# Kernel optimization log

Hardware: AMD Instinct MI355X
Metric: run time of the kernel (lower is better)

The kernel has to match this reference:

```python
import jax, jax.numpy as jnp
import numpy as np
from jax import lax

# ---- geometry (from Mamba2PoSTMixer defaults + chosen d_model) ----
D_MODEL = 1024
EXPAND = 2
HEADDIM = 64
D_STATE = 128
D_CONV = 4
CHUNK = 256
D_INNER = EXPAND * D_MODEL            # 2048
NHEADS = D_INNER // HEADDIM           # 32
D_CONV_CH = D_INNER + 2 * D_STATE     # conv acts on x, B, C
D_IN_PROJ = 2 * D_INNER + 2 * D_STATE + NHEADS
BATCH, SEQLEN = 2, 4096
EPS = 1e-5


def setup_inputs() -> dict:
    key = jax.random.key(0)
    ks = jax.random.split(key, 8)
    f = jnp.float32
    return {
        "hidden_states": jax.random.normal(ks[0], (BATCH, SEQLEN, D_MODEL), f),
        "residual": jax.random.normal(ks[1], (BATCH, SEQLEN, D_MODEL), f),
        "norm_weight": jnp.ones((D_MODEL,), f),
        "in_proj_w": jax.random.normal(ks[2], (D_MODEL, D_IN_PROJ), f) * 0.02,
        "conv_w": jax.random.normal(ks[3], (D_CONV, 1, D_CONV_CH), f) * 0.2,  # WIO, depthwise
        "conv_b": jnp.zeros((D_CONV_CH,), f),
        "dt_bias": jnp.log(jnp.expm1(jax.random.uniform(ks[4], (NHEADS,), f, 1e-3, 1e-1))),
        "A_log": jnp.log(jax.random.uniform(ks[5], (NHEADS,), f, 1.0, 16.0)),
        "D": jnp.ones((NHEADS,), f),
        "gate_norm_weight": jnp.ones((D_INNER,), f),
        "out_proj_w": jax.random.normal(ks[6], (D_INNER, D_MODEL), f) * 0.02,
    }


def _rmsnorm(x, w, eps=EPS):
    return x * lax.rsqrt(jnp.mean(x * x, axis=-1, keepdims=True) + eps) * w


def _segsum(x):
    # x: [..., T] -> [..., T, T] lower-triangular cumulative segment sums
    T = x.shape[-1]
    cs = jnp.cumsum(x, axis=-1)
    ss = cs[..., :, None] - cs[..., None, :]
    mask = jnp.tril(jnp.ones((T, T), bool))
    return jnp.where(mask, ss, -jnp.inf)


def _ssd(xdt, dtA, Bm, Cm):
    # xdt: [b,l,h,p] (x already scaled by dt), dtA: [b,l,h], Bm/Cm: [b,l,n]
    b, l, h, p = xdt.shape
    n = Bm.shape[-1]
    c = l // CHUNK
    x = xdt.reshape(b, c, CHUNK, h, p)
    A = dtA.reshape(b, c, CHUNK, h).transpose(0, 3, 1, 2)     # [b,h,c,l]
    Bc = Bm.reshape(b, c, CHUNK, n)
    Cc = Cm.reshape(b, c, CHUNK, n)
    A_cum = jnp.cumsum(A, axis=-1)                            # [b,h,c,l]
    # intra-chunk (diagonal block) output
    L = jnp.exp(_segsum(A))                                   # [b,h,c,l,s]
    Y_diag = jnp.einsum('bcln,bcsn,bhcls,bcshp->bclhp', Cc, Bc, L, x)
    # per-chunk final states
    decay_states = jnp.exp(A_cum[..., -1:] - A_cum)           # [b,h,c,l]
    states = jnp.einsum('bcln,bhcl,bclhp->bchpn', Bc, decay_states, x)
    # inter-chunk recurrence over chunk states
    chunk_decay = jnp.exp(A_cum[..., -1])                     # [b,h,c]
    def step(carry, inp):
        dec, s = inp                                          # dec: [b,h], s: [b,h,p,n]
        return carry * dec[..., None, None] + s, carry
    init = jnp.zeros((b, h, p, n), xdt.dtype)
    _, prev = lax.scan(step, init,
                       (jnp.moveaxis(chunk_decay, -1, 0), jnp.moveaxis(states, 1, 0)))
    prev = jnp.moveaxis(prev, 0, 1)                           # [b,c,h,p,n] states entering each chunk
    Y_off = jnp.einsum('bcln,bchpn,bhcl->bclhp', Cc, prev, jnp.exp(A_cum))
    return (Y_diag + Y_off).reshape(b, l, h, p)


def reference(hidden_states, residual, norm_weight, in_proj_w, conv_w, conv_b,
              dt_bias, A_log, D, gate_norm_weight, out_proj_w):
    # residual add + RMSNorm (Mamba2PoSTBlock)
    res = hidden_states + residual
    h = _rmsnorm(res, norm_weight)
    # Mamba2 mixer
    zxbcdt = h @ in_proj_w                                    # [b,l, 2*Di + 2*N + H]
    z, xBC, dt_raw = jnp.split(zxbcdt, [D_INNER, D_INNER + D_CONV_CH], axis=-1)
    # depthwise causal conv over (x, B, C) channels + SiLU
    xp = jnp.pad(xBC, ((0, 0), (D_CONV - 1, 0), (0, 0)))
    xBC = lax.conv_general_dilated(xp, conv_w, (1,), 'VALID',
                                   dimension_numbers=('NWC', 'WIO', 'NWC'),
                                   feature_group_count=D_CONV_CH) + conv_b
    xBC = jax.nn.silu(xBC)
    x, Bm, Cm = jnp.split(xBC, [D_INNER, D_INNER + D_STATE], axis=-1)
    dt = jax.nn.softplus(dt_raw + dt_bias)                    # [b,l,H]
    A = -jnp.exp(A_log)                                       # [H]
    xh = x.reshape(x.shape[0], x.shape[1], NHEADS, HEADDIM)   # [b,l,h,p]
    y = _ssd(xh * dt[..., None], dt * A, Bm, Cm)
    y = y + D[None, None, :, None] * xh                       # skip (D) term
    y = y.reshape(y.shape[0], y.shape[1], D_INNER)
    y = _rmsnorm(y * jax.nn.silu(z), gate_norm_weight)        # gated RMSNorm
    out = y @ out_proj_w
    return out, res
```

## Files before the change

kernel.cpp:

```cpp
#include <hip/hip_runtime.h>
#include <hip/hip_bf16.h>
#include <math.h>

#define BATCH   2
#define LQ      4096
#define RTOT    8192
#define DM      1024
#define DI      2048
#define NH      32
#define HD      64
#define DS      128
#define CH      256
#define NC      16
#define XBC_C   2304
#define ZX_C    4384
#define ZXS     4352
#define NP1     4480
#define EPS     1e-5f
#define LOG2E   1.4426950408889634f

typedef __hip_bfloat16 bf16;
typedef __bf16 bf16x8v __attribute__((ext_vector_type(8)));
typedef __bf16 bf16x4v __attribute__((ext_vector_type(4)));
typedef float f32x4v __attribute__((ext_vector_type(4)));

__device__ __forceinline__ float block_reduce_sum(float v) {
    __shared__ float sred[8];
    int lane = threadIdx.x & 63, w = threadIdx.x >> 6;
#pragma unroll
    for (int off = 32; off > 0; off >>= 1) v += __shfl_down(v, off, 64);
    if (lane == 0) sred[w] = v;
    __syncthreads();
    float t = (threadIdx.x < (int)(blockDim.x >> 6)) ? sred[threadIdx.x] : 0.f;
    if (w == 0) {
#pragma unroll
        for (int off = 4; off > 0; off >>= 1) t += __shfl_down(t, off, 64);
        if (lane == 0) sred[0] = t;
    }
    __syncthreads();
    return sred[0];
}

__device__ __forceinline__ void transpose_tile(
    const float* __restrict__ W, bf16* __restrict__ WT, int K, int N,
    int n0, int k0) {
    __shared__ float t[32][33];
    int tx = threadIdx.x & 31, ty = threadIdx.x >> 5;
#pragma unroll
    for (int r = 0; r < 32; r += 8) {
        int k = k0 + ty + r, n = n0 + tx;
        t[ty + r][tx] = (n < N) ? W[(size_t)k * N + n] : 0.f;
    }
    __syncthreads();
#pragma unroll
    for (int r = 0; r < 32; r += 8) {
        int n = n0 + ty + r, k = k0 + tx;
        WT[(size_t)n * K + k] = __float2bfloat16(t[tx][ty + r]);
    }
}

__global__ __launch_bounds__(256) void fused_pre_kernel(
    const float* __restrict__ hid, const float* __restrict__ resid,
    const float* __restrict__ w, float* __restrict__ res_out,
    bf16* __restrict__ h_out, const float* __restrict__ in_proj,
    bf16* __restrict__ Bt1) {
    int bid = blockIdx.x;
    if (bid < RTOT) {
        int r = bid, tid = threadIdx.x;
        size_t base = (size_t)r * DM;
        float4 hv = *(const float4*)&hid[base + tid * 4];
        float4 rv = *(const float4*)&resid[base + tid * 4];
        float4 s = {hv.x + rv.x, hv.y + rv.y, hv.z + rv.z, hv.w + rv.w};
        *(float4*)&res_out[base + tid * 4] = s;
        float ss = s.x * s.x + s.y * s.y + s.z * s.z + s.w * s.w;
        ss = block_reduce_sum(ss);
        float scale = rsqrtf(ss / (float)DM + EPS);
        float4 wv = *(const float4*)&w[tid * 4];
        __hip_bfloat162 p0, p1;
        p0.x = __float2bfloat16(s.x * scale * wv.x);
        p0.y = __float2bfloat16(s.y * scale * wv.y);
        p1.x = __float2bfloat16(s.z * scale * wv.z);
        p1.y = __float2bfloat16(s.w * scale * wv.w);
        bf16* hp = &h_out[base + tid * 4];
        *(__hip_bfloat162*)hp = p0;
        *(__hip_bfloat162*)(hp + 2) = p1;
    } else {
        int t = bid - RTOT;
        transpose_tile(in_proj, Bt1, DM, ZX_C, (t % 140) * 32, (t / 140) * 32);
    }
}

template <int WRITE_F32>
__global__ __launch_bounds__(256) void gemm_mfma_kernel(
    const bf16* __restrict__ A, int lda, const bf16* __restrict__ Bt,
    void* __restrict__ C, int ldc, int M, int N, int K,
    float* __restrict__ dtraw) {
    __shared__ __align__(16) bf16 As[128 * 32];
    __shared__ __align__(16) bf16 Bs[128 * 32];
    int tid = threadIdx.x;
    int lane = tid & 63, wave = tid >> 6;
    int wm = (wave >> 1) * 64, wn = (wave & 1) * 64;
    int m0 = blockIdx.y * 128, n0 = blockIdx.x * 128;
    int fr = lane & 15, kg = lane >> 4;

    int off0 = tid * 16, off1 = off0 + 4096;
    int row0 = off0 >> 6, colb0 = off0 & 63;
    int row1 = off1 >> 6, colb1 = off1 & 63;
    const bf16* ga0 = A + (size_t)(m0 + row0) * lda + (colb0 >> 1);
    const bf16* ga1 = A + (size_t)(m0 + row1) * lda + (colb1 >> 1);
    const bf16* gb0 = Bt + (size_t)(n0 + row0) * K + (colb0 >> 1);
    const bf16* gb1 = Bt + (size_t)(n0 + row1) * K + (colb1 >> 1);

    f32x4v acc[4][4] = {};
    for (int k0 = 0; k0 < K; k0 += 32) {
        __syncthreads();
        __builtin_amdgcn_global_load_lds(
            (const __attribute__((address_space(1))) void*)(ga0 + k0),
            (__attribute__((address_space(3))) void*)((char*)As + off0), 16, 0, 0);
        __builtin_amdgcn_global_load_lds(
            (const __attribute__((address_space(1))) void*)(ga1 + k0),
            (__attribute__((address_space(3))) void*)((char*)As + off1), 16, 0, 0);
        __builtin_amdgcn_global_load_lds(
            (const __attribute__((address_space(1))) void*)(gb0 + k0),
            (__attribute__((address_space(3))) void*)((char*)Bs + off0), 16, 0, 0);
        __builtin_amdgcn_global_load_lds(
            (const __attribute__((address_space(1))) void*)(gb1 + k0),
            (__attribute__((address_space(3))) void*)((char*)Bs + off1), 16, 0, 0);
        __syncthreads();
        bf16x8v af[4], bfv[4];
#pragma unroll
        for (int mt = 0; mt < 4; ++mt)
            af[mt] = *(const bf16x8v*)&As[(wm + mt * 16 + fr) * 32 + kg * 8];
#pragma unroll
        for (int nt = 0; nt < 4; ++nt)
            bfv[nt] = *(const bf16x8v*)&Bs[(wn + nt * 16 + fr) * 32 + kg * 8];
#pragma unroll
        for (int mt = 0; mt < 4; ++mt)
#pragma unroll
            for (int nt = 0; nt < 4; ++nt)
                acc[mt][nt] = __builtin_amdgcn_mfma_f32_16x16x32_bf16(
                    af[mt], bfv[nt], acc[mt][nt], 0, 0, 0);
    }
    int col = lane & 15, rbase = (lane >> 4) * 4;
#pragma unroll
    for (int mt = 0; mt < 4; ++mt) {
#pragma unroll
        for (int nt = 0; nt < 4; ++nt) {
            int gn = n0 + wn + nt * 16 + col;
            if (gn >= N) continue;
#pragma unroll
            for (int rg = 0; rg < 4; ++rg) {
                int gm = m0 + wm + mt * 16 + rbase + rg;
                float v = acc[mt][nt][rg];
                if (WRITE_F32) {
                    ((float*)C)[(size_t)gm * ldc + gn] = v;
                } else {
                    if (gn < 4352)
                        ((bf16*)C)[(size_t)gm * ldc + gn] = __float2bfloat16(v);
                    else if (dtraw)
                        dtraw[(size_t)gm * 32 + (gn - 4352)] = v;
                }
            }
        }
    }
}

__global__ __launch_bounds__(256) void fused_conv_dt_kernel(
    const bf16* __restrict__ zx, const float* __restrict__ conv_w,
    const float* __restrict__ conv_b, bf16* __restrict__ xBC,
    const float* __restrict__ dtraw, const float* __restrict__ dt_bias,
    const float* __restrict__ A_log, float* __restrict__ dt_bh,
    float* __restrict__ Ac2_bh) {
    int bid = blockIdx.x;
    if (bid < 9216) {
        int idx = bid * 256 + threadIdx.x;
        int r = idx / 288;
        int o = idx - r * 288;
        int c = o * 8;
        int b = r >> 12, l = r & (LQ - 1);
        float acc[8];
        {
            float4 cb0 = *(const float4*)&conv_b[c];
            float4 cb1 = *(const float4*)&conv_b[c + 4];
            acc[0] = cb0.x; acc[1] = cb0.y; acc[2] = cb0.z; acc[3] = cb0.w;
            acc[4] = cb1.x; acc[5] = cb1.y; acc[6] = cb1.z; acc[7] = cb1.w;
        }
#pragma unroll
        for (int k = 0; k < 4; ++k) {
            int t = l - 3 + k;
            if (t >= 0) {
                bf16x8v xv = *(const bf16x8v*)&zx[(size_t)(b * LQ + t) * ZXS + DI + c];
                float4 w0 = *(const float4*)&conv_w[k * XBC_C + c];
                float4 w1 = *(const float4*)&conv_w[k * XBC_C + c + 4];
                acc[0] = fmaf(w0.x, (float)xv[0], acc[0]);
                acc[1] = fmaf(w0.y, (float)xv[1], acc[1]);
                acc[2] = fmaf(w0.z, (float)xv[2], acc[2]);
                acc[3] = fmaf(w0.w, (float)xv[3], acc[3]);
                acc[4] = fmaf(w1.x, (float)xv[4], acc[4]);
                acc[5] = fmaf(w1.y, (float)xv[5], acc[5]);
                acc[6] = fmaf(w1.z, (float)xv[6], acc[6]);
                acc[7] = fmaf(w1.w, (float)xv[7], acc[7]);
            }
        }
        bf16x8v ov;
#pragma unroll
        for (int j = 0; j < 8; ++j)
            ov[j] = (__bf16)(acc[j] / (1.f + __expf(-acc[j])));
        *(bf16x8v*)&xBC[(size_t)r * XBC_C + c] = ov;
    } else {
        __shared__ float sA[256];
        int b2 = bid - 9216;
        int c = b2 & 15, h = (b2 >> 4) & 31, b = b2 >> 9;
        int tid = threadIdx.x;
        int l = c * CH + tid;
        int r = b * LQ + l;
        float v = dtraw[(size_t)r * 32 + h] + dt_bias[h];
        float dt = (v > 20.f) ? v : log1pf(expf(v));
        float A = -expf(A_log[h]);
        sA[tid] = dt * A * LOG2E;
        __syncthreads();
        for (int off = 1; off < 256; off <<= 1) {
            float t = (tid >= off) ? sA[tid - off] : 0.f;
            __syncthreads();
            sA[tid] += t;
            __syncthreads();
        }
        size_t o = (size_t)(b * NH + h) * LQ + l;
        dt_bh[o] = dt;
        Ac2_bh[o] = sA[tid];
    }
}

__global__ __launch_bounds__(256) void states_mfma_kernel(
    const bf16* __restrict__ xBC, const float* __restrict__ dt_bh,
    const float* __restrict__ Ac2, float* __restrict__ states) {
    __shared__ __align__(16) __bf16 xdT[64][264];
    __shared__ __align__(16) __bf16 BT[64][264];
    int bid = blockIdx.x;
    int c = bid & 15, h = (bid >> 4) & 31, b = bid >> 9;
    int bh = b * NH + h;
    int rch = b * LQ + c * CH;
    int tid = threadIdx.x;
    int wave = tid >> 6, lane = tid & 63;
    int fr = lane & 15, kg = lane >> 4;
    float Ac2last = Ac2[(size_t)bh * LQ + c * CH + (CH - 1)];

    {
        int p2 = (tid & 31) * 2;
        int srow = tid >> 5;
#pragma unroll 4
        for (int pass = 0; pass < 32; ++pass) {
            int s = pass * 8 + srow;
            float sc = dt_bh[(size_t)bh * LQ + c * CH + s] *
                       exp2f(Ac2last - Ac2[(size_t)bh * LQ + c * CH + s]);
            __hip_bfloat162 xv =
                *(const __hip_bfloat162*)&xBC[(size_t)(rch + s) * XBC_C + h * HD + p2];
            xdT[p2][s]     = (__bf16)(__bfloat162float(xv.x) * sc);
            xdT[p2 + 1][s] = (__bf16)(__bfloat162float(xv.y) * sc);
        }
    }
    int wm = (wave >> 1) * 32, wn = (wave & 1) * 32;
    size_t base = (size_t)(bh * NC + c) * HD * DS;
    for (int nh = 0; nh < 2; ++nh) {
        __syncthreads();
        {
            int n_oct = tid & 7, lrow = tid >> 3;
#pragma unroll
            for (int pass = 0; pass < 8; ++pass) {
                int l = pass * 32 + lrow;
                bf16x8v bv = *(const bf16x8v*)
                    &xBC[(size_t)(rch + l) * XBC_C + DI + nh * 64 + n_oct * 8];
#pragma unroll
                for (int j = 0; j < 8; ++j)
                    BT[n_oct * 8 + j][l] = bv[j];
            }
        }
        __syncthreads();
        f32x4v acc[2][2] = {};
#pragma unroll
        for (int kb = 0; kb < 8; ++kb) {
            bf16x8v A2[2], B2[2];
#pragma unroll
            for (int i = 0; i < 2; ++i)
                A2[i] = *(const bf16x8v*)&xdT[wm + i * 16 + fr][kb * 32 + kg * 8];
#pragma unroll
            for (int j = 0; j < 2; ++j)
                B2[j] = *(const bf16x8v*)&BT[wn + j * 16 + fr][kb * 32 + kg * 8];
#pragma unroll
            for (int i = 0; i < 2; ++i)
#pragma unroll
                for (int j = 0; j < 2; ++j)
                    acc[i][j] = __builtin_amdgcn_mfma_f32_16x16x32_bf16(
                        A2[i], B2[j], acc[i][j], 0, 0, 0);
        }
#pragma unroll
        for (int i = 0; i < 2; ++i)
#pragma unroll
            for (int j = 0; j < 2; ++j)
#pragma unroll
                for (int rg = 0; rg < 4; ++rg) {
                    int p = wm + i * 16 + kg * 4 + rg;
                    int n = nh * 64 + wn + j * 16 + fr;
                    states[base + (size_t)p * DS + n] = acc[i][j][rg];
                }
    }
}

__global__ __launch_bounds__(256) void chunk_scan_kernel(
    float* __restrict__ states, const float* __restrict__ Ac2) {
    int bh = blockIdx.x;
    int tid = threadIdx.x;
    float carry[32];
#pragma unroll
    for (int j = 0; j < 32; ++j) carry[j] = 0.f;
    for (int c = 0; c < NC; ++c) {
        float dec = exp2f(Ac2[(size_t)bh * LQ + c * CH + (CH - 1)]);
        size_t base = (size_t)(bh * NC + c) * (HD * DS);
#pragma unroll
        for (int j = 0; j < 32; ++j) {
            size_t idx = base + tid + j * 256;
            float tmp = states[idx];
            states[idx] = carry[j];
            carry[j] = carry[j] * dec + tmp;
        }
    }
}

template <int MASKED>
__device__ __forceinline__ void y_slab(
    const bf16* __restrict__ xBC, int rch, int s0, int fr, int kg,
    const float* As_sh, const float* Al, const bf16x8v CA[4][4],
    __bf16 (*Pw)[36], const __bf16 (*xdtT)[264], f32x4v accY[4][4]) {
#pragma unroll
    for (int half = 0; half < 2; ++half) {
        f32x4v Sacc[2][4] = {};
#pragma unroll
        for (int ks = 0; ks < 4; ++ks) {
            bf16x8v SB[2];
#pragma unroll
            for (int st2 = 0; st2 < 2; ++st2)
                SB[st2] = *(const bf16x8v*)&xBC[
                    (size_t)(rch + s0 + half * 32 + st2 * 16 + fr) * XBC_C
                    + DI + ks * 32 + kg * 8];
#pragma unroll
            for (int st2 = 0; st2 < 2; ++st2)
#pragma unroll
                for (int mt = 0; mt < 4; ++mt) {
                    if (MASKED && (half * 2 + st2) > mt) continue;
                    Sacc[st2][mt] = __builtin_amdgcn_mfma_f32_16x16x32_bf16(
                        SB[st2], CA[mt][ks], Sacc[st2][mt], 0, 0, 0);
                }
        }
#pragma unroll
        for (int st2 = 0; st2 < 2; ++st2) {
            int sblk = half * 2 + st2;
            float4 As4 = *(const float4*)&As_sh[s0 + half * 32 + st2 * 16 + kg * 4];
            float as[4] = {As4.x, As4.y, As4.z, As4.w};
#pragma unroll
            for (int mt = 0; mt < 4; ++mt) {
                bf16x4v pv;
                if (MASKED && sblk > mt) {
                    pv[0] = pv[1] = pv[2] = pv[3] = (__bf16)0.f;
                } else {
#pragma unroll
                    for (int rg = 0; rg < 4; ++rg) {
                        float v = Sacc[st2][mt][rg] * exp2f(Al[mt] - as[rg]);
                        if (MASKED && sblk == mt && (kg * 4 + rg) > fr) v = 0.f;
                        pv[rg] = (__bf16)v;
                    }
                }
                *(bf16x4v*)&Pw[mt * 16 + fr][st2 * 16 + kg * 4] = pv;
            }
        }
        __asm__ volatile("s_waitcnt lgkmcnt(0)" ::: "memory");
        bf16x8v PA[4], XB[4];
#pragma unroll
        for (int mt = 0; mt < 4; ++mt) {
            bf16x4v plo = *(const bf16x4v*)&Pw[mt * 16 + fr][kg * 8];
            bf16x4v phi = *(const bf16x4v*)&Pw[mt * 16 + fr][kg * 8 + 4];
            bf16x8v pa;
#pragma unroll
            for (int j = 0; j < 4; ++j) { pa[j] = plo[j]; pa[4 + j] = phi[j]; }
            PA[mt] = pa;
        }
#pragma unroll
        for (int pt = 0; pt < 4; ++pt)
            XB[pt] = *(const bf16x8v*)&xdtT[pt * 16 + fr][s0 + half * 32 + kg * 8];
#pragma unroll
        for (int mt = 0; mt < 4; ++mt)
#pragma unroll
            for (int pt = 0; pt < 4; ++pt)
                accY[mt][pt] = __builtin_amdgcn_mfma_f32_16x16x32_bf16(
                    PA[mt], XB[pt], accY[mt][pt], 0, 0, 0);
        __asm__ volatile("s_waitcnt lgkmcnt(0)" ::: "memory");
    }
}

__global__ __launch_bounds__(256) void y_mfma_kernel(
    const bf16* __restrict__ xBC, const float* __restrict__ dt_bh,
    const float* __restrict__ Ac2, const float* __restrict__ prev,
    bf16* __restrict__ yout ) {
    __shared__ __align__(16) __bf16 xdtT[64][264];
    __shared__ __align__(16) __bf16 P[4][64][36];
    __shared__ float As_sh[256];
    int bid = blockIdx.x;
    int c = bid & 15, h = (bid >> 4) & 31, b = bid >> 9;
    int bh = b * NH + h;
    int rch = b * LQ + c * CH;
    int tid = threadIdx.x;
    int wave = tid >> 6, lane = tid & 63;
    int fr = lane & 15, kg = lane >> 4;

    As_sh[tid] = Ac2[(size_t)bh * LQ + c * CH + tid];
    {
        int p2 = (tid & 31) * 2;
        int srow = tid >> 5;
#pragma unroll 4
        for (int pass = 0; pass < 32; ++pass) {
            int s = pass * 8 + srow;
            float dtv = dt_bh[(size_t)bh * LQ + c * CH + s];
            __hip_bfloat162 xv =
                *(const __hip_bfloat162*)&xBC[(size_t)(rch + s) * XBC_C + h * HD + p2];
            xdtT[p2][s]     = (__bf16)(__bfloat162float(xv.x) * dtv);
            xdtT[p2 + 1][s] = (__bf16)(__bfloat162float(xv.y) * dtv);
        }
    }
    __syncthreads();

    bf16x8v CA[4][4];
    {
        size_t rb = (size_t)(rch + wave * 64 + fr) * XBC_C + DI + DS + kg * 8;
#pragma unroll
        for (int mt = 0; mt < 4; ++mt)
#pragma unroll
            for (int ks = 0; ks < 4; ++ks)
                CA[mt][ks] = *(const bf16x8v*)&xBC[rb + (size_t)mt * 16 * XBC_C + ks * 32];
    }

    f32x4v accY[4][4] = {};

    {
        size_t pbase = (size_t)(bh * NC + c) * HD * DS;
#pragma unroll
        for (int ks = 0; ks < 4; ++ks) {
            bf16x8v PB[4];
#pragma unroll
            for (int pt = 0; pt < 4; ++pt) {
                const float* pp = &prev[pbase + (size_t)(pt * 16 + fr) * DS + ks * 32 + kg * 8];
                float4 a4 = *(const float4*)pp;
                float4 b4 = *(const float4*)(pp + 4);
                bf16x8v t;
                t[0] = (__bf16)a4.x; t[1] = (__bf16)a4.y; t[2] = (__bf16)a4.z; t[3] = (__bf16)a4.w;
                t[4] = (__bf16)b4.x; t[5] = (__bf16)b4.y; t[6] = (__bf16)b4.z; t[7] = (__bf16)b4.w;
                PB[pt] = t;
            }
#pragma unroll
            for (int mt = 0; mt < 4; ++mt)
#pragma unroll
                for (int pt = 0; pt < 4; ++pt)
                    accY[mt][pt] = __builtin_amdgcn_mfma_f32_16x16x32_bf16(
                        CA[mt][ks], PB[pt], accY[mt][pt], 0, 0, 0);
        }
    }
    int l0 = wave * 64;
#pragma unroll
    for (int mt = 0; mt < 4; ++mt) {
#pragma unroll
        for (int rg = 0; rg < 4; ++rg) {
            float e = exp2f(As_sh[l0 + mt * 16 + kg * 4 + rg]);
#pragma unroll
            for (int pt = 0; pt < 4; ++pt)
                accY[mt][pt][rg] *= e;
        }
    }

    float Al[4];
#pragma unroll
    for (int mt = 0; mt < 4; ++mt) Al[mt] = As_sh[l0 + mt * 16 + fr];

    __bf16 (*Pw)[36] = P[wave];
    for (int st = 0; st < wave; ++st)
        y_slab<0>(xBC, rch, st * 64, fr, kg, As_sh, Al, CA, Pw, xdtT, accY);
    y_slab<1>(xBC, rch, l0, fr, kg, As_sh, Al, CA, Pw, xdtT, accY);

#pragma unroll
    for (int ph = 0; ph < 2; ++ph) {
#pragma unroll
        for (int mt = 0; mt < 4; ++mt)
#pragma unroll
            for (int ptl = 0; ptl < 2; ++ptl)
#pragma unroll
                for (int rg = 0; rg < 4; ++rg)
                    Pw[mt * 16 + kg * 4 + rg][ptl * 16 + fr] =
                        (__bf16)accY[mt][ph * 2 + ptl][rg];
        __asm__ volatile("s_waitcnt lgkmcnt(0)" ::: "memory");
        bf16* yp = yout + (size_t)(rch + l0 + lane) * ZXS + h * HD + ph * 32;
#pragma unroll
        for (int q = 0; q < 4; ++q) {
            bf16x4v a = *(const bf16x4v*)&Pw[lane][q * 8];
            bf16x4v bq = *(const bf16x4v*)&Pw[lane][q * 8 + 4];
            bf16x8v v;
#pragma unroll
            for (int j = 0; j < 4; ++j) { v[j] = a[j]; v[4 + j] = bq[j]; }
            *(bf16x8v*)(yp + q * 8) = v;
        }
        __asm__ volatile("s_waitcnt lgkmcnt(0)" ::: "memory");
    }
}

__global__ __launch_bounds__(256) void fused_gate_trans_kernel(
    const bf16* __restrict__ zx, const float* __restrict__ gw,
    const float* __restrict__ Dvec, const bf16* __restrict__ xBC,
    bf16* __restrict__ y ,
    const float* __restrict__ out_proj, bf16* __restrict__ Bt2) {
    int bid = blockIdx.x;
    if (bid < RTOT) {
        int r = bid, tid = threadIdx.x;
        int i0 = tid * 8;
        bf16x8v zv = *(const bf16x8v*)&zx[(size_t)r * ZXS + i0];
        bf16x8v yv = *(const bf16x8v*)&y[(size_t)r * ZXS + i0];
        bf16x8v xv = *(const bf16x8v*)&xBC[(size_t)r * XBC_C + i0];
        float Dh = Dvec[tid >> 3];
        float v[8];
        float ss = 0.f;
#pragma unroll
        for (int j = 0; j < 8; ++j) {
            float z = (float)zv[j];
            float val = ((float)yv[j] + Dh * (float)xv[j]) * (z / (1.f + __expf(-z)));
            v[j] = val;
            ss += val * val;
        }
        ss = block_reduce_sum(ss);
        float scale = rsqrtf(ss / (float)DI + EPS);
        float4 g0 = *(const float4*)&gw[i0];
        float4 g1 = *(const float4*)&gw[i0 + 4];
        float g[8] = {g0.x, g0.y, g0.z, g0.w, g1.x, g1.y, g1.z, g1.w};
        bf16x8v ov;
#pragma unroll
        for (int j = 0; j < 8; ++j)
            ov[j] = (__bf16)(v[j] * scale * g[j]);
        *(bf16x8v*)&y[(size_t)r * ZXS + i0] = ov;
    } else {
        int t = bid - RTOT;
        transpose_tile(out_proj, Bt2, DI, DM, (t & 31) * 32, (t >> 5) * 32);
    }
}

extern "C" void kernel_launch(void* const* d_in, const int* in_sizes, int n_in,
                              void* d_out, int out_size, void* d_ws, size_t ws_size,
                              hipStream_t stream) {
    const float* hid      = (const float*)d_in[0];
    const float* resid    = (const float*)d_in[1];
    const float* norm_w   = (const float*)d_in[2];
    const float* in_proj  = (const float*)d_in[3];
    const float* conv_w   = (const float*)d_in[4];
    const float* conv_b   = (const float*)d_in[5];
    const float* dt_bias  = (const float*)d_in[6];
    const float* A_log    = (const float*)d_in[7];
    const float* Dvec     = (const float*)d_in[8];
    const float* gate_w   = (const float*)d_in[9];
    const float* out_proj = (const float*)d_in[10];

    float* out_p   = (float*)d_out;
    float* res_out = out_p + (size_t)RTOT * DM;
    bf16*  h_bf16  = (bf16*)out_p;
    float* states  = out_p;

    char* wsb = (char*)d_ws;
    bf16*  zx      = (bf16*)wsb;  wsb += (size_t)RTOT * ZXS * sizeof(bf16);
    bf16*  xBC     = (bf16*)wsb;  wsb += (size_t)RTOT * XBC_C * sizeof(bf16);
    float* dtraw   = (float*)wsb; wsb += (size_t)RTOT * 32 * sizeof(float);
    float* dt_bh   = (float*)wsb; wsb += (size_t)BATCH * NH * LQ * sizeof(float);
    float* Ac2_bh  = (float*)wsb; wsb += (size_t)BATCH * NH * LQ * sizeof(float);
    wsb += (size_t)1 << 20;
    bf16* Bt1 = xBC;
    bf16* Bt2 = (bf16*)dtraw;

    fused_pre_kernel<<<RTOT + 4480, 256, 0, stream>>>(
        hid, resid, norm_w, res_out, h_bf16, in_proj, Bt1);
    gemm_mfma_kernel<0><<<dim3(NP1 / 128, RTOT / 128), 256, 0, stream>>>(
        h_bf16, DM, Bt1, zx, ZXS, RTOT, ZX_C, DM, dtraw);
    fused_conv_dt_kernel<<<9216 + 1024, 256, 0, stream>>>(
        zx, conv_w, conv_b, xBC, dtraw, dt_bias, A_log, dt_bh, Ac2_bh);
    states_mfma_kernel<<<BATCH * NH * NC, 256, 0, stream>>>(
        xBC, dt_bh, Ac2_bh, states);
    chunk_scan_kernel<<<BATCH * NH, 256, 0, stream>>>(states, Ac2_bh);
    y_mfma_kernel<<<BATCH * NH * NC, 256, 0, stream>>>(
        xBC, dt_bh, Ac2_bh, states, zx + DI);
    fused_gate_trans_kernel<<<RTOT + 2048, 256, 0, stream>>>(
        zx, gate_w, Dvec, xBC, zx + DI, out_proj, Bt2);
    gemm_mfma_kernel<1><<<dim3(DM / 128, RTOT / 128), 256, 0, stream>>>(
        zx + DI, ZXS, Bt2, out_p, DM, RTOT, DM, DI, nullptr);
}
```

Baseline: 529.8 us.

## Replace GEMM with 256-row, 8-wave, double-buffered, swizzled 8-phase pipelined MFMA kernel

Both projection GEMMs move from a simple 128x128 tile kernel, which synchronises twice per 32-wide K step, to a 256xBN tile kernel with 512 threads. It double-buffers 64-wide K tiles in LDS with XOR-swizzled layout and interleaves async global-to-LDS loads with MFMA phases under explicit waitcnt and barrier control. It also raises MFMA priority and swizzles the block order for L2 reuse. The in_proj N padding grows to 4608, so the transpose and grid sizes change, and a bounds check guards the dtraw writes. The aim is better MFMA utilisation and latency hiding, at the cost of higher LDS and register use and fragile hand-tuned vmcnt counts.

```diff
diff --git a/kernel.cpp b/kernel.cpp
--- a/kernel.cpp
+++ b/kernel.cpp
@@ -15,7 +15,7 @@
 #define XBC_C   2304
 #define ZX_C    4384
 #define ZXS     4352
-#define NP1     4480
+#define NP1     4608
 #define EPS     1e-5f
 #define LOG2E   1.4426950408889634f
 
@@ -86,78 +86,174 @@
         *(__hip_bfloat162*)(hp + 2) = p1;
     } else {
         int t = bid - RTOT;
-        transpose_tile(in_proj, Bt1, DM, ZX_C, (t % 140) * 32, (t / 140) * 32);
-    }
-}
-
-template <int WRITE_F32>
-__global__ __launch_bounds__(256) void gemm_mfma_kernel(
-    const bf16* __restrict__ A, int lda, const bf16* __restrict__ Bt,
-    void* __restrict__ C, int ldc, int M, int N, int K,
-    float* __restrict__ dtraw) {
-    __shared__ __align__(16) bf16 As[128 * 32];
-    __shared__ __align__(16) bf16 Bs[128 * 32];
-    int tid = threadIdx.x;
-    int lane = tid & 63, wave = tid >> 6;
-    int wm = (wave >> 1) * 64, wn = (wave & 1) * 64;
-    int m0 = blockIdx.y * 128, n0 = blockIdx.x * 128;
-    int fr = lane & 15, kg = lane >> 4;
-
-    int off0 = tid * 16, off1 = off0 + 4096;
-    int row0 = off0 >> 6, colb0 = off0 & 63;
-    int row1 = off1 >> 6, colb1 = off1 & 63;
-    const bf16* ga0 = A + (size_t)(m0 + row0) * lda + (colb0 >> 1);
-    const bf16* ga1 = A + (size_t)(m0 + row1) * lda + (colb1 >> 1);
-    const bf16* gb0 = Bt + (size_t)(n0 + row0) * K + (colb0 >> 1);
-    const bf16* gb1 = Bt + (size_t)(n0 + row1) * K + (colb1 >> 1);
-
-    f32x4v acc[4][4] = {};
-    for (int k0 = 0; k0 < K; k0 += 32) {
-        __syncthreads();
-        __builtin_amdgcn_global_load_lds(
-            (const __attribute__((address_space(1))) void*)(ga0 + k0),
-            (__attribute__((address_space(3))) void*)((char*)As + off0), 16, 0, 0);
-        __builtin_amdgcn_global_load_lds(
-            (const __attribute__((address_space(1))) void*)(ga1 + k0),
-            (__attribute__((address_space(3))) void*)((char*)As + off1), 16, 0, 0);
-        __builtin_amdgcn_global_load_lds(
-            (const __attribute__((address_space(1))) void*)(gb0 + k0),
-            (__attribute__((address_space(3))) void*)((char*)Bs + off0), 16, 0, 0);
-        __builtin_amdgcn_global_load_lds(
-            (const __attribute__((address_space(1))) void*)(gb1 + k0),
-            (__attribute__((address_space(3))) void*)((char*)Bs + off1), 16, 0, 0);
-        __syncthreads();
-        bf16x8v af[4], bfv[4];
-#pragma unroll
-        for (int mt = 0; mt < 4; ++mt)
-            af[mt] = *(const bf16x8v*)&As[(wm + mt * 16 + fr) * 32 + kg * 8];
-#pragma unroll
-        for (int nt = 0; nt < 4; ++nt)
-            bfv[nt] = *(const bf16x8v*)&Bs[(wn + nt * 16 + fr) * 32 + kg * 8];
-#pragma unroll
-        for (int mt = 0; mt < 4; ++mt)
-#pragma unroll
-            for (int nt = 0; nt < 4; ++nt)
-                acc[mt][nt] = __builtin_amdgcn_mfma_f32_16x16x32_bf16(
-                    af[mt], bfv[nt], acc[mt][nt], 0, 0, 0);
-    }
-    int col = lane & 15, rbase = (lane >> 4) * 4;
-#pragma unroll
-    for (int mt = 0; mt < 4; ++mt) {
-#pragma unroll
-        for (int nt = 0; nt < 4; ++nt) {
-            int gn = n0 + wn + nt * 16 + col;
-            if (gn >= N) continue;
+        transpose_tile(in_proj, Bt1, DM, ZX_C, (t % 144) * 32, (t / 144) * 32);
+    }
+}
+
+#define GFENCE asm volatile("" ::: "memory")
+#define GBAR do { GFENCE; __builtin_amdgcn_s_barrier(); GFENCE; } while (0)
+#define GWAIT_LGKM                                                             \
+    do {                                                                       \
+        asm volatile("s_waitcnt lgkmcnt(0)" ::: "memory");                     \
+        __builtin_amdgcn_sched_barrier(0);                                     \
+    } while (0)
+#define GWAIT_VM0 asm volatile("s_waitcnt vmcnt(0)" ::: "memory")
+#define GWAIT_VMN                                                              \
+    do {                                                                       \
+        if constexpr (BN == 256)                                               \
+            asm volatile("s_waitcnt vmcnt(6)" ::: "memory");                   \
+        else                                                                   \
+            asm volatile("s_waitcnt vmcnt(4)" ::: "memory");                   \
+    } while (0)
+
+#define RD_A(buf, ml)                                                          \
+    do {                                                                       \
+        _Pragma("unroll") for (int mt_ = 0; mt_ < 4; ++mt_)                    \
+        _Pragma("unroll") for (int kk_ = 0; kk_ < 2; ++kk_)                    \
+            aF[mt_][kk_] = *(const bf16x8v*)&As[buf][                          \
+                (wm * 128 + ((ml) * 4 + mt_) * 16 + fr) * 64 +                 \
+                ((((kk_ << 2) | kg) ^ s7) << 3)];                              \
+    } while (0)
+
+#define RD_B(buf)                                                              \
+    do {                                                                       \
+        _Pragma("unroll") for (int nt_ = 0; nt_ < NTW; ++nt_)                  \
+        _Pragma("unroll") for (int kk_ = 0; kk_ < 2; ++kk_)                    \
+            bF[nt_][kk_] = *(const bf16x8v*)&Bs[buf][                          \
+                (wn * (BN / 4) + nt_ * 16 + fr) * 64 +                         \
+                ((((kk_ << 2) | kg) ^ s7) << 3)];                              \
+    } while (0)
+
+#define QMFMA(ml, nl)                                                          \
+    do {                                                                       \
+        __builtin_amdgcn_s_setprio(1);                                         \
+        _Pragma("unroll") for (int mt_ = 0; mt_ < 4; ++mt_)                    \
+        _Pragma("unroll") for (int nt_ = 0; nt_ < NTH; ++nt_)                  \
+        _Pragma("unroll") for (int kk_ = 0; kk_ < 2; ++kk_)                    \
+            acc[(ml) * 4 + mt_][(nl) * NTH + nt_] =                            \
+                __builtin_amdgcn_mfma_f32_16x16x32_bf16(                       \
+                    aF[mt_][kk_], bF[(nl) * NTH + nt_][kk_],                   \
+                    acc[(ml) * 4 + mt_][(nl) * NTH + nt_], 0, 0, 0);           \
+        __builtin_amdgcn_s_setprio(0);                                         \
+    } while (0)
+
+template <int BN, int WRITE_F32>
+__global__ __launch_bounds__(512, 2) void gemm_8ph_kernel(
+    const bf16* __restrict__ A, int lda, const bf16* __restrict__ Bt, int ldb,
+    void* __restrict__ C, int ldc, int NXT, int K, float* __restrict__ dtraw) {
+    constexpr int BM = 256;
+    constexpr int NTW = BN / 64;
+    constexpr int NTH = NTW / 2;
+    constexpr int BLOADS = BN / 128;
+    __shared__ __align__(16) bf16 As[2][BM * 64];
+    __shared__ __align__(16) bf16 Bs[2][BN * 64];
+
+    const int tid = threadIdx.x;
+    const int lane = tid & 63;
+    const int wave = tid >> 6;
+    const int wm = wave >> 2, wn = wave & 3;
+    const int fr = lane & 15, kg = lane >> 4;
+    const int s7 = fr & 7;
+
+    const int bid = blockIdx.x;
+    const int swz = (bid & 7) * ((int)gridDim.x >> 3) + (bid >> 3);
+    const int mtile = swz / NXT;
+    const int m0 = mtile * BM;
+    const int n0 = (swz - mtile * NXT) * BN;
+
+    const int trow = tid >> 3;
+    const int scol = ((tid & 7) ^ (trow & 7)) << 3;
+    const bf16* aSrc = A + (size_t)(m0 + trow) * lda + scol;
+    const bf16* bSrc = Bt + (size_t)(n0 + trow) * ldb + scol;
+
+    auto stageA = [&](int kt, int h) {
+#pragma unroll
+        for (int j = 0; j < 2; ++j)
+            __builtin_amdgcn_global_load_lds(
+                (const __attribute__((address_space(1))) void*)(
+                    aSrc + (size_t)(h * 128 + j * 64) * lda + kt * 64),
+                (__attribute__((address_space(3))) void*)(
+                    &As[kt & 1][(h * 128 + j * 64) * 64 + tid * 8]),
+                16, 0, 0);
+    };
+    auto stageB = [&](int kt, int h) {
+#pragma unroll
+        for (int j = 0; j < BLOADS; ++j)
+            __builtin_amdgcn_global_load_lds(
+                (const __attribute__((address_space(1))) void*)(
+                    bSrc + (size_t)(h * (BN / 2) + j * 64) * ldb + kt * 64),
+                (__attribute__((address_space(3))) void*)(
+                    &Bs[kt & 1][(h * (BN / 2) + j * 64) * 64 + tid * 8]),
+                16, 0, 0);
+    };
+
+    f32x4v acc[8][NTW] = {};
+    bf16x8v aF[4][2], bF[NTW][2];
+
+    stageB(0, 0); stageB(0, 1); stageA(0, 0); stageA(0, 1);
+    stageB(1, 0); stageB(1, 1); stageA(1, 0);
+    GWAIT_VMN;
+    GBAR;
+
+    const int NIT = K >> 7;
+    for (int t = 0; t < NIT; ++t) {
+        const int k1 = 2 * t + 1, k2 = 2 * t + 2, k3 = 2 * t + 3;
+        const bool full = (t < NIT - 1);
+        RD_B(0); RD_A(0, 0);
+        stageA(k1, 1);
+        GBAR; GWAIT_LGKM;
+        QMFMA(0, 0);
+        GBAR;
+        if (full) stageB(k2, 0);
+        GBAR;
+        QMFMA(0, 1);
+        GBAR;
+        RD_A(0, 1);
+        if (full) stageB(k2, 1);
+        GBAR; GWAIT_LGKM;
+        QMFMA(1, 0);
+        GBAR;
+        if (full) stageA(k2, 0);
+        GBAR;
+        QMFMA(1, 1);
+        if (full) { GWAIT_VMN; } else { GWAIT_VM0; }
+        GBAR;
+        RD_B(1); RD_A(1, 0);
+        if (full) stageA(k2, 1);
+        GBAR; GWAIT_LGKM;
+        QMFMA(0, 0);
+        GBAR;
+        if (full) stageB(k3, 0);
+        GBAR;
+        QMFMA(0, 1);
+        GBAR;
+        RD_A(1, 1);
+        if (full) stageB(k3, 1);
+        GBAR; GWAIT_LGKM;
+        QMFMA(1, 0);
+        GBAR;
+        if (full) stageA(k3, 0);
+        GBAR;
+        QMFMA(1, 1);
+        if (full) { GWAIT_VMN; }
+        GBAR;
+    }
+
+#pragma unroll
+    for (int mt = 0; mt < 8; ++mt) {
+#pragma unroll
+        for (int nt = 0; nt < NTW; ++nt) {
+            int gn = n0 + wn * (BN / 4) + nt * 16 + fr;
 #pragma unroll
             for (int rg = 0; rg < 4; ++rg) {
-                int gm = m0 + wm + mt * 16 + rbase + rg;
+                int gm = m0 + wm * 128 + mt * 16 + kg * 4 + rg;
                 float v = acc[mt][nt][rg];
                 if (WRITE_F32) {
                     ((float*)C)[(size_t)gm * ldc + gn] = v;
                 } else {
                     if (gn < 4352)
                         ((bf16*)C)[(size_t)gm * ldc + gn] = __float2bfloat16(v);
-                    else if (dtraw)
+                    else if (gn < 4384)
                         dtraw[(size_t)gm * 32 + (gn - 4352)] = v;
                 }
             }
@@ -576,10 +672,10 @@
     bf16* Bt1 = xBC;
     bf16* Bt2 = (bf16*)dtraw;
 
-    fused_pre_kernel<<<RTOT + 4480, 256, 0, stream>>>(
+    fused_pre_kernel<<<RTOT + 4608, 256, 0, stream>>>(
         hid, resid, norm_w, res_out, h_bf16, in_proj, Bt1);
-    gemm_mfma_kernel<0><<<dim3(NP1 / 128, RTOT / 128), 256, 0, stream>>>(
-        h_bf16, DM, Bt1, zx, ZXS, RTOT, ZX_C, DM, dtraw);
+    gemm_8ph_kernel<256, 0><<<576, 512, 0, stream>>>(
+        h_bf16, DM, Bt1, DM, zx, ZXS, 18, DM, dtraw);
     fused_conv_dt_kernel<<<9216 + 1024, 256, 0, stream>>>(
         zx, conv_w, conv_b, xBC, dtraw, dt_bias, A_log, dt_bh, Ac2_bh);
     states_mfma_kernel<<<BATCH * NH * NC, 256, 0, stream>>>(
@@ -589,6 +685,6 @@
         xBC, dt_bh, Ac2_bh, states, zx + DI);
     fused_gate_trans_kernel<<<RTOT + 2048, 256, 0, stream>>>(
         zx, gate_w, Dvec, xBC, zx + DI, out_proj, Bt2);
-    gemm_mfma_kernel<1><<<dim3(DM / 128, RTOT / 128), 256, 0, stream>>>(
-        zx + DI, ZXS, Bt2, out_p, DM, RTOT, DM, DI, nullptr);
-}
+    gemm_8ph_kernel<128, 1><<<256, 512, 0, stream>>>(
+        zx + DI, ZXS, Bt2, DI, out_p, DM, 8, DI, nullptr);
+}
```

Measured after the change: 498.9 us. 5.8% less time.
